# Performance work log

Hardware: AMD Instinct MI355X
Metric: run time of the kernel (lower is better)

Reference implementation:

```python
import jax, jax.numpy as jnp
import numpy as np

D_IN = 768   # raw feature dim
D = 256      # encoded dim (from nn.Linear(256*2, 1))


def setup_inputs() -> dict:
    key = jax.random.key(0)
    ks = jax.random.split(key, 8)
    B = 4096
    images = jax.random.normal(ks[0], (B, D_IN), jnp.float32)
    texts = jax.random.normal(ks[1], (B, D_IN), jnp.float32)
    s = 1.0 / np.sqrt(D_IN)
    W_img = jax.random.normal(ks[2], (D_IN, D), jnp.float32) * s
    b_img = jnp.zeros((D,), jnp.float32)
    W_txt = jax.random.normal(ks[3], (D_IN, D), jnp.float32) * s
    b_txt = jnp.zeros((D,), jnp.float32)
    cs_w = jax.random.normal(ks[4], (2 * D, 1), jnp.float32) / np.sqrt(2 * D)
    cs_b = jnp.zeros((1,), jnp.float32)
    # dense [B,B] stand-in for the discovery edge_weights dict
    edge_weights = jax.random.uniform(ks[5], (B, B), jnp.float32)
    return {"images": images, "texts": texts, "W_img": W_img, "b_img": b_img,
            "W_txt": W_txt, "b_txt": b_txt, "cs_w": cs_w, "cs_b": cs_b,
            "edge_weights": edge_weights}


def reference(images, texts, W_img, b_img, W_txt, b_txt, cs_w, cs_b, edge_weights):
    # encoders (Definition.encode_*) + suppress_modality (identity)
    img_f = images @ W_img + b_img            # [B, D]
    text_f = texts @ W_txt + b_txt            # [B, D]

    # cosine similarity: matmul normalized by per-row norms
    sim = img_f @ text_f.T                    # [B, B]
    norm_img = jnp.linalg.norm(img_f, axis=1, keepdims=True)   # [B,1]
    norm_text = jnp.linalg.norm(text_f, axis=1, keepdims=True) # [B,1]
    sim = sim / (norm_img @ norm_text.T)

    # causal strength: Linear(concat(img_f[i], text_f[j])) decomposes as
    # img_f @ w1 + text_f @ w2 + b, then outer-broadcast over (i, j)
    w1, w2 = cs_w[:D], cs_w[D:]               # [D,1] each
    strength = (img_f @ w1) + (text_f @ w2).T + cs_b  # [B, B]
    causal = edge_weights * strength

    final = sim + 0.3 * causal
    return final, sim, causal
```

## Files before the change

### kernel.cpp

```cpp
#include <hip/hip_runtime.h>
#include <hip/hip_bf16.h>

typedef __bf16 bf16_t;
typedef __bf16 bf16x8 __attribute__((ext_vector_type(8)));
typedef float f32x4 __attribute__((ext_vector_type(4)));

typedef __attribute__((address_space(3))) void lds_void;
typedef __attribute__((address_space(1))) void gbl_void;

static constexpr int NB  = 4096;
static constexpr int KIN = 768;
static constexpr int DD  = 256;
static constexpr int FS  = NB * 32;

__global__ __launch_bounds__(256) void pack_wt_kernel(
    const float* __restrict__ Wi, const float* __restrict__ Wx,
    bf16_t* __restrict__ Oi, bf16_t* __restrict__ Ox)
{
  __shared__ bf16_t tile[64][66];
  const int b = blockIdx.x;
  const bool isTxt = (b >= 48);
  const int t = isTxt ? b - 48 : b;
  const float* W = isTxt ? Wx : Wi;
  bf16_t* O      = isTxt ? Ox : Oi;
  const int k0 = (t % 12) * 64;
  const int c0 = (t / 12) * 64;
  const int cl = threadIdx.x & 63;
  const int rw = threadIdx.x >> 6;

#pragma unroll
  for (int p = 0; p < 16; ++p) {
    const int kl = p * 4 + rw;
    tile[kl][cl] = (bf16_t)W[(size_t)(k0 + kl) * DD + c0 + cl];
  }
  __syncthreads();
#pragma unroll
  for (int p = 0; p < 16; ++p) {
    const int clo = p * 4 + rw;
    const int col = c0 + clo;
    const int k   = k0 + cl;
    O[(size_t)(k >> 5) * 8192 + col * 32 + (k & 31)] = tile[cl][clo];
  }
}

__global__ __launch_bounds__(256) void proj_kernel(
    const float* __restrict__ images, const float* __restrict__ texts,
    const bf16_t* __restrict__ Wti, const bf16_t* __restrict__ Wtt,
    const float* __restrict__ b_img, const float* __restrict__ b_txt,
    const float* __restrict__ cs_w,
    bf16_t* __restrict__ Fi, bf16_t* __restrict__ Ft,
    float* __restrict__ rni, float* __restrict__ si,
    float* __restrict__ rnt, float* __restrict__ st)
{
  __shared__ float xs[16 * KIN];
  __shared__ float lnsq[4][16];
  __shared__ float lsdt[4][16];

  const int bid = blockIdx.x;
  const bool isTxt = (bid >= 256);
  const float* X    = isTxt ? texts : images;
  const bf16_t* Wt  = isTxt ? Wtt : Wti;
  const float* bias = isTxt ? b_txt : b_img;
  const float* csw  = cs_w + (isTxt ? DD : 0);
  bf16_t* F     = isTxt ? Ft : Fi;
  float* rnorm  = isTxt ? rnt : rni;
  float* svec   = isTxt ? st : si;

  const int tid  = threadIdx.x;
  const int lane = tid & 63;
  const int wave = tid >> 6;
  const int lrow = lane & 15;
  const int g    = lane >> 4;
  const int rb   = (bid & 255) * 16;
  const int cwb  = wave * 64;

#pragma unroll
  for (int i = 0; i < 12; ++i) {
    const int U   = wave * 768 + i * 64 + lane;
    const int row = U / 192;
    const int su  = U - row * 192;
    const int ou  = su ^ (row & 7);
    const float* gp = X + (size_t)(rb + row) * KIN + ou * 4;
    char* lb = (char*)xs + wave * 12288 + i * 1024;
    __builtin_amdgcn_global_load_lds((const gbl_void*)gp, (lds_void*)lb, 16, 0, 0);
  }
  __syncthreads();

  const f32x4 fzero = {0.f, 0.f, 0.f, 0.f};
  f32x4 acc[4];
#pragma unroll
  for (int n = 0; n < 4; ++n) acc[n] = fzero;

  const bf16_t* wtb  = Wt + (size_t)(cwb + lrow) * 32 + g * 8;
  const float*  xrow = xs + lrow * KIN;
  const int     rsw  = lrow & 7;

#pragma unroll 4
  for (int ks = 0; ks < KIN / 32; ++ks) {
    const int u0 = ks * 8 + g * 2;
    f32x4 x0 = *reinterpret_cast<const f32x4*>(xrow + ((u0    ) ^ rsw) * 4);
    f32x4 x1 = *reinterpret_cast<const f32x4*>(xrow + ((u0 + 1) ^ rsw) * 4);
    bf16x8 a;
#pragma unroll
    for (int e = 0; e < 4; ++e) { a[e] = (bf16_t)x0[e]; a[e + 4] = (bf16_t)x1[e]; }
#pragma unroll
    for (int n = 0; n < 4; ++n) {
      bf16x8 bfr = *reinterpret_cast<const bf16x8*>(wtb + ks * 8192 + n * 512);
      acc[n] = __builtin_amdgcn_mfma_f32_16x16x32_bf16(a, bfr, acc[n], 0, 0, 0);
    }
  }

  float nsq[4] = {0.f, 0.f, 0.f, 0.f};
  float sdt[4] = {0.f, 0.f, 0.f, 0.f};
#pragma unroll
  for (int n = 0; n < 4; ++n) {
    const int col = cwb + n * 16 + lrow;
    const float bn = bias[col];
    const float wn = csw[col];
    const size_t cbase = (size_t)(col >> 5) * FS + (col & 31);
#pragma unroll
    for (int r = 0; r < 4; ++r) {
      float v = acc[n][r] + bn;
      const int row = rb + g * 4 + r;
      F[cbase + row * 32] = (bf16_t)v;
      nsq[r] += v * v;
      sdt[r] += v * wn;
    }
  }
#pragma unroll
  for (int msk = 8; msk >= 1; msk >>= 1) {
#pragma unroll
    for (int r = 0; r < 4; ++r) {
      nsq[r] += __shfl_xor(nsq[r], msk, 64);
      sdt[r] += __shfl_xor(sdt[r], msk, 64);
    }
  }
  if (lrow == 0) {
#pragma unroll
    for (int r = 0; r < 4; ++r) {
      lnsq[wave][g * 4 + r] = nsq[r];
      lsdt[wave][g * 4 + r] = sdt[r];
    }
  }
  __syncthreads();
  if (tid < 16) {
    float tn = 0.f, ts = 0.f;
#pragma unroll
    for (int w2 = 0; w2 < 4; ++w2) { tn += lnsq[w2][tid]; ts += lsdt[w2][tid]; }
    rnorm[rb + tid] = 1.0f / sqrtf(tn);
    svec [rb + tid] = ts;
  }
}

__global__ __launch_bounds__(256, 2) void sim_kernel(
    const bf16_t* __restrict__ Fi, const bf16_t* __restrict__ Ft,
    const float* __restrict__ rni, const float* __restrict__ si,
    const float* __restrict__ rnt, const float* __restrict__ st,
    const float* __restrict__ cs_b, const float* __restrict__ edge,
    float* __restrict__ out_final, float* __restrict__ out_sim,
    float* __restrict__ out_causal)
{
  extern __shared__ float smem[];

  const int bid = blockIdx.x;
  const int swz = (bid & 7) * 128 + (bid >> 3);
  const int bx = swz & 31;
  const int by = swz >> 5;

  const int tid  = threadIdx.x;
  const int lane = tid & 63;
  const int wave = tid >> 6;
  const int wr = wave >> 1;
  const int wc = wave & 1;
  const int lrow = lane & 15;
  const int g    = lane >> 4;

  const int rowG0 = by * 128;
  const int colG0 = bx * 128;
  const int rowBase = rowG0 + wr * 64;
  const int colBase = colG0 + wc * 64;

  f32x4 ewr[16];
#pragma unroll
  for (int it = 0; it < 16; ++it) {
    const int e = (it * 256 + tid) * 4;
    const int r = e >> 7;
    const int c = e & 127;
    ewr[it] = __builtin_nontemporal_load(
        reinterpret_cast<const f32x4*>(edge + (size_t)(rowG0 + r) * NB + colG0 + c));
  }
  asm volatile("" ::: "memory");

  const f32x4 fzero = {0.f, 0.f, 0.f, 0.f};
  f32x4 acc[4][4];
#pragma unroll
  for (int m = 0; m < 4; ++m)
#pragma unroll
    for (int n = 0; n < 4; ++n) acc[m][n] = fzero;

  const size_t arow = (size_t)(rowBase + lrow) * 32 + g * 8;
  const size_t brow = (size_t)(colBase + lrow) * 32 + g * 8;

#pragma unroll 2
  for (int ks = 0; ks < DD / 32; ++ks) {
    const size_t so = (size_t)ks * FS;
    bf16x8 a[4], b[4];
#pragma unroll
    for (int m = 0; m < 4; ++m)
      a[m] = *reinterpret_cast<const bf16x8*>(Fi + so + arow + m * 512);
#pragma unroll
    for (int n = 0; n < 4; ++n)
      b[n] = *reinterpret_cast<const bf16x8*>(Ft + so + brow + n * 512);
#pragma unroll
    for (int m = 0; m < 4; ++m)
#pragma unroll
      for (int n = 0; n < 4; ++n)
        acc[m][n] = __builtin_amdgcn_mfma_f32_16x16x32_bf16(a[m], b[n], acc[m][n], 0, 0, 0);
  }

  float rntv[4];
#pragma unroll
  for (int n = 0; n < 4; ++n) rntv[n] = rnt[colBase + n * 16 + lrow];
  float rnv[4][4];
#pragma unroll
  for (int m = 0; m < 4; ++m)
#pragma unroll
    for (int r = 0; r < 4; ++r) rnv[m][r] = rni[rowBase + m * 16 + g * 4 + r];

#pragma unroll
  for (int m = 0; m < 4; ++m) {
#pragma unroll
    for (int n = 0; n < 4; ++n) {
#pragma unroll
      for (int r = 0; r < 4; ++r) {
        const int rl = wr * 64 + m * 16 + g * 4 + r;
        const int cl = wc * 64 + n * 16 + lrow;
        smem[rl * 128 + (cl ^ ((rl & 7) << 2))] = acc[m][n][r] * rnv[m][r] * rntv[n];
      }
    }
  }
  __syncthreads();

  const float cb = cs_b[0];
#pragma unroll
  for (int it = 0; it < 16; ++it) {
    const int e = (it * 256 + tid) * 4;
    const int r = e >> 7;
    const int c = e & 127;
    const f32x4 sv4 = *reinterpret_cast<const f32x4*>(&smem[r * 128 + (c ^ ((r & 7) << 2))]);
    const float sir = si[rowG0 + r];
    const f32x4 st4 = *reinterpret_cast<const f32x4*>(st + colG0 + c);
    const size_t idx = (size_t)(rowG0 + r) * NB + colG0 + c;
    f32x4 ca4, fin4;
#pragma unroll
    for (int j = 0; j < 4; ++j) {
      const float strength = sir + st4[j] + cb;
      ca4[j]  = ewr[it][j] * strength;
      fin4[j] = sv4[j] + 0.3f * ca4[j];
    }
    *reinterpret_cast<f32x4*>(out_sim    + idx) = sv4;
    *reinterpret_cast<f32x4*>(out_causal + idx) = ca4;
    *reinterpret_cast<f32x4*>(out_final  + idx) = fin4;
  }
}

extern "C" void kernel_launch(void* const* d_in, const int* in_sizes, int n_in,
                              void* d_out, int out_size, void* d_ws, size_t ws_size,
                              hipStream_t stream) {
  const float* images = (const float*)d_in[0];
  const float* texts  = (const float*)d_in[1];
  const float* W_img  = (const float*)d_in[2];
  const float* b_img  = (const float*)d_in[3];
  const float* W_txt  = (const float*)d_in[4];
  const float* b_txt  = (const float*)d_in[5];
  const float* cs_w   = (const float*)d_in[6];
  const float* cs_b   = (const float*)d_in[7];
  const float* edge   = (const float*)d_in[8];

  float* out_final  = (float*)d_out;
  float* out_sim    = out_final + (size_t)NB * NB;
  float* out_causal = out_sim   + (size_t)NB * NB;

  char* ws = (char*)d_ws;
  bf16_t* Fi  = (bf16_t*)ws;
  bf16_t* Ft  = Fi  + (size_t)NB * DD;
  bf16_t* Wti = Ft  + (size_t)NB * DD;
  bf16_t* Wtt = Wti + (size_t)DD * KIN;
  float*  rni = (float*)(Wtt + (size_t)DD * KIN);
  float*  siv = rni + NB;
  float*  rnt = siv + NB;
  float*  stv = rnt + NB;

  pack_wt_kernel<<<96, 256, 0, stream>>>(W_img, W_txt, Wti, Wtt);
  proj_kernel<<<512, 256, 0, stream>>>(images, texts, Wti, Wtt, b_img, b_txt, cs_w,
                                       Fi, Ft, rni, siv, rnt, stv);
  sim_kernel<<<1024, 256, 65536, stream>>>(Fi, Ft, rni, siv, rnt, stv, cs_b, edge,
                                           out_final, out_sim, out_causal);
}
```

Measured before the change: 81.48 us.

## Halve sim_kernel LDS staging and drop edge prefetch to raise occupancy

The sim kernel now writes its 128x128 output tile through a 32 KB static LDS buffer in two 64-row halves instead of a 64 KB dynamic buffer. The edge-weight tile is no longer prefetched into 16 registers before the MFMA loop; it is loaded inside the epilogue. Launch bounds go from 2 to 4 blocks per CU, and the A-fragment rows are remapped so each half holds rows from both row-waves. The goal is higher occupancy to hide memory latency, at the cost of losing the edge-load overlap with the matmul and adding an extra barrier.

Result: slower. 85.11 us (+4.5%).

```diff
diff --git a/kernel.cpp b/kernel.cpp
--- a/kernel.cpp
+++ b/kernel.cpp
@@ -152,7 +152,7 @@
   }
 }
 
-__global__ __launch_bounds__(256, 2) void sim_kernel(
+__global__ __launch_bounds__(256, 4) void sim_kernel(
     const bf16_t* __restrict__ Fi, const bf16_t* __restrict__ Ft,
     const float* __restrict__ rni, const float* __restrict__ si,
     const float* __restrict__ rnt, const float* __restrict__ st,
@@ -160,7 +160,7 @@
     float* __restrict__ out_final, float* __restrict__ out_sim,
     float* __restrict__ out_causal)
 {
-  extern __shared__ float smem[];
+  __shared__ float smem[64 * 128];
 
   const int bid = blockIdx.x;
   const int swz = (bid & 7) * 128 + (bid >> 3);
@@ -177,19 +177,7 @@
 
   const int rowG0 = by * 128;
   const int colG0 = bx * 128;
-  const int rowBase = rowG0 + wr * 64;
   const int colBase = colG0 + wc * 64;
-
-  f32x4 ewr[16];
-#pragma unroll
-  for (int it = 0; it < 16; ++it) {
-    const int e = (it * 256 + tid) * 4;
-    const int r = e >> 7;
-    const int c = e & 127;
-    ewr[it] = __builtin_nontemporal_load(
-        reinterpret_cast<const f32x4*>(edge + (size_t)(rowG0 + r) * NB + colG0 + c));
-  }
-  asm volatile("" ::: "memory");
 
   const f32x4 fzero = {0.f, 0.f, 0.f, 0.f};
   f32x4 acc[4][4];
@@ -198,16 +186,18 @@
 #pragma unroll
     for (int n = 0; n < 4; ++n) acc[m][n] = fzero;
 
-  const size_t arow = (size_t)(rowBase + lrow) * 32 + g * 8;
-  const size_t brow = (size_t)(colBase + lrow) * 32 + g * 8;
+  const size_t arowL = (size_t)(rowG0 + wr * 32 + lrow) * 32 + g * 8;
+  const size_t brow  = (size_t)(colBase + lrow) * 32 + g * 8;
 
 #pragma unroll 2
   for (int ks = 0; ks < DD / 32; ++ks) {
     const size_t so = (size_t)ks * FS;
     bf16x8 a[4], b[4];
 #pragma unroll
-    for (int m = 0; m < 4; ++m)
-      a[m] = *reinterpret_cast<const bf16x8*>(Fi + so + arow + m * 512);
+    for (int m = 0; m < 4; ++m) {
+      const int h = m >> 1, m2 = m & 1;
+      a[m] = *reinterpret_cast<const bf16x8*>(Fi + so + arowL + h * 2048 + m2 * 512);
+    }
 #pragma unroll
     for (int n = 0; n < 4; ++n)
       b[n] = *reinterpret_cast<const bf16x8*>(Ft + so + brow + n * 512);
@@ -218,49 +208,56 @@
         acc[m][n] = __builtin_amdgcn_mfma_f32_16x16x32_bf16(a[m], b[n], acc[m][n], 0, 0, 0);
   }
 
+  const float cb = cs_b[0];
   float rntv[4];
 #pragma unroll
   for (int n = 0; n < 4; ++n) rntv[n] = rnt[colBase + n * 16 + lrow];
-  float rnv[4][4];
-#pragma unroll
-  for (int m = 0; m < 4; ++m)
-#pragma unroll
-    for (int r = 0; r < 4; ++r) rnv[m][r] = rni[rowBase + m * 16 + g * 4 + r];
-
-#pragma unroll
-  for (int m = 0; m < 4; ++m) {
-#pragma unroll
-    for (int n = 0; n < 4; ++n) {
-#pragma unroll
-      for (int r = 0; r < 4; ++r) {
-        const int rl = wr * 64 + m * 16 + g * 4 + r;
+
+#pragma unroll
+  for (int h = 0; h < 2; ++h) {
+#pragma unroll
+    for (int m2 = 0; m2 < 2; ++m2) {
+      const int m = h * 2 + m2;
+      const int rbase = wr * 32 + m2 * 16 + g * 4;
+      float rn[4];
+#pragma unroll
+      for (int r = 0; r < 4; ++r) rn[r] = rni[rowG0 + h * 64 + rbase + r];
+#pragma unroll
+      for (int n = 0; n < 4; ++n) {
         const int cl = wc * 64 + n * 16 + lrow;
-        smem[rl * 128 + (cl ^ ((rl & 7) << 2))] = acc[m][n][r] * rnv[m][r] * rntv[n];
+#pragma unroll
+        for (int r = 0; r < 4; ++r) {
+          const int rl = rbase + r;
+          smem[rl * 128 + (cl ^ ((rl & 7) << 2))] = acc[m][n][r] * rn[r] * rntv[n];
+        }
       }
     }
-  }
-  __syncthreads();
-
-  const float cb = cs_b[0];
-#pragma unroll
-  for (int it = 0; it < 16; ++it) {
-    const int e = (it * 256 + tid) * 4;
-    const int r = e >> 7;
-    const int c = e & 127;
-    const f32x4 sv4 = *reinterpret_cast<const f32x4*>(&smem[r * 128 + (c ^ ((r & 7) << 2))]);
-    const float sir = si[rowG0 + r];
-    const f32x4 st4 = *reinterpret_cast<const f32x4*>(st + colG0 + c);
-    const size_t idx = (size_t)(rowG0 + r) * NB + colG0 + c;
-    f32x4 ca4, fin4;
-#pragma unroll
-    for (int j = 0; j < 4; ++j) {
-      const float strength = sir + st4[j] + cb;
-      ca4[j]  = ewr[it][j] * strength;
-      fin4[j] = sv4[j] + 0.3f * ca4[j];
-    }
-    *reinterpret_cast<f32x4*>(out_sim    + idx) = sv4;
-    *reinterpret_cast<f32x4*>(out_causal + idx) = ca4;
-    *reinterpret_cast<f32x4*>(out_final  + idx) = fin4;
+    __syncthreads();
+
+#pragma unroll
+    for (int it = 0; it < 8; ++it) {
+      const int e  = (it * 256 + tid) * 4;
+      const int r0 = e >> 7;
+      const int c  = e & 127;
+      const int grow = rowG0 + h * 64 + r0;
+      const size_t idx = (size_t)grow * NB + colG0 + c;
+      const f32x4 ew4 = __builtin_nontemporal_load(
+          reinterpret_cast<const f32x4*>(edge + idx));
+      const f32x4 sv4 = *reinterpret_cast<const f32x4*>(&smem[r0 * 128 + (c ^ ((r0 & 7) << 2))]);
+      const float sir = si[grow];
+      const f32x4 st4 = *reinterpret_cast<const f32x4*>(st + colG0 + c);
+      f32x4 ca4, fin4;
+#pragma unroll
+      for (int j = 0; j < 4; ++j) {
+        const float strength = sir + st4[j] + cb;
+        ca4[j]  = ew4[j] * strength;
+        fin4[j] = sv4[j] + 0.3f * ca4[j];
+      }
+      *reinterpret_cast<f32x4*>(out_sim    + idx) = sv4;
+      *reinterpret_cast<f32x4*>(out_causal + idx) = ca4;
+      *reinterpret_cast<f32x4*>(out_final  + idx) = fin4;
+    }
+    if (h == 0) __syncthreads();
   }
 }
 
@@ -294,6 +291,6 @@
   pack_wt_kernel<<<96, 256, 0, stream>>>(W_img, W_txt, Wti, Wtt);
   proj_kernel<<<512, 256, 0, stream>>>(images, texts, Wti, Wtt, b_img, b_txt, cs_w,
                                        Fi, Ft, rni, siv, rnt, stv);
-  sim_kernel<<<1024, 256, 65536, stream>>>(Fi, Ft, rni, siv, rnt, stv, cs_b, edge,
-                                           out_final, out_sim, out_causal);
-}
+  sim_kernel<<<1024, 256, 0, stream>>>(Fi, Ft, rni, siv, rnt, stv, cs_b, edge,
+                                       out_final, out_sim, out_causal);
+}
```
